# Kernel optimization log

Hardware: AMD Instinct MI355X
Metric: run time of the kernel (lower is better)

Reference implementation:

```python
import jax, jax.numpy as jnp
import numpy as np

B, S, D = 4, 2048, 1024
H, HD = 16, 64

def setup_inputs() -> dict:
    key = jax.random.key(0)
    ks = jax.random.split(key, 5)
    scale = 1.0 / np.sqrt(D)
    return {
        "x": jax.random.normal(ks[0], (B, S, D), dtype=jnp.float32),
        "Wq": jax.random.normal(ks[1], (D, D), dtype=jnp.float32) * scale,
        "Wk": jax.random.normal(ks[2], (D, D), dtype=jnp.float32) * scale,
        "Wv": jax.random.normal(ks[3], (D, D), dtype=jnp.float32) * scale,
        "Wo": jax.random.normal(ks[4], (D, D), dtype=jnp.float32) * scale,
        "bo": jnp.zeros((D,), dtype=jnp.float32),
    }

def reference(x, Wq, Wk, Wv, Wo, bo):
    batch, tokens, _ = x.shape
    # Linear weights applied as x @ W^T to match torch nn.Linear; here W is [out,in] equiv square
    q = (x @ Wq).reshape(batch, tokens, H, HD).transpose(0, 2, 1, 3)  # [B,H,S,HD]
    k = (x @ Wk).reshape(batch, tokens, H, HD).transpose(0, 2, 1, 3)
    v = (x @ Wv).reshape(batch, tokens, H, HD).transpose(0, 2, 1, 3)
    scores = jnp.einsum('bhqd,bhkd->bhqk', q, k) / jnp.sqrt(jnp.float32(HD))
    causal = jnp.tril(jnp.ones((tokens, tokens), dtype=bool))  # True = keep
    scores = jnp.where(causal[None, None], scores, -jnp.inf)
    attn = jax.nn.softmax(scores, axis=-1)  # dropout is identity (eval / rate 0)
    ctx = jnp.einsum('bhqk,bhkd->bhqd', attn, v)
    ctx = ctx.transpose(0, 2, 1, 3).reshape(batch, tokens, D)
    return ctx @ Wo + bo
```

## Files before the change

kernel.cpp:

```cpp
#include <hip/hip_runtime.h>
#include <math.h>
#include <stdint.h>

constexpr int kB = 4;
constexpr int kS = 2048;
constexpr int kD = 1024;
constexpr int kH = 16;
constexpr int kHD = 64;

typedef __bf16 bf16;
typedef __attribute__((ext_vector_type(4))) __bf16 bf16x4;
typedef __attribute__((ext_vector_type(8))) __bf16 bf16x8;
typedef __attribute__((ext_vector_type(4))) float f32x4;

__device__ __forceinline__ f32x4 mfma16x16x32(bf16x8 a, bf16x8 b, f32x4 c) {
    return __builtin_amdgcn_mfma_f32_16x16x32_bf16(a, b, c, 0, 0, 0);
}

#if __has_builtin(__builtin_amdgcn_exp2f)
#define EXP2F(x) __builtin_amdgcn_exp2f(x)
#else
#define EXP2F(x) exp2f(x)
#endif

__device__ __forceinline__ void load_lds16(const bf16* g, bf16* lds) {
    __builtin_amdgcn_global_load_lds(
        (const __attribute__((address_space(1))) void*)g,
        (__attribute__((address_space(3))) void*)lds, 16, 0, 0);
}

__global__ __launch_bounds__(256) void prep_x(const float* __restrict__ x,
                                              bf16* __restrict__ xb) {
    size_t i = ((size_t)blockIdx.x * 256 + threadIdx.x) * 8;
    float4 f0 = *(const float4*)(x + i);
    float4 f1 = *(const float4*)(x + i + 4);
    bf16x8 v;
    v[0] = (bf16)f0.x; v[1] = (bf16)f0.y; v[2] = (bf16)f0.z; v[3] = (bf16)f0.w;
    v[4] = (bf16)f1.x; v[5] = (bf16)f1.y; v[6] = (bf16)f1.z; v[7] = (bf16)f1.w;
    *(bf16x8*)(xb + i) = v;
}

__global__ __launch_bounds__(256) void prep_w(const float* __restrict__ Wq,
                                              const float* __restrict__ Wk,
                                              const float* __restrict__ Wv,
                                              const float* __restrict__ Wo,
                                              bf16* __restrict__ Wt) {
    __shared__ bf16 t[64 * 72];
    const int z = blockIdx.z;
    const float* W = (z == 0) ? Wq : (z == 1) ? Wk : (z == 2) ? Wv : Wo;
    const float scale = (z == 0) ? 0.18033688011112042f : 1.0f;
    const int k0 = blockIdx.x * 64, n0 = blockIdx.y * 64;
    const int tid = threadIdx.x;
    for (int p = 0; p < 16; ++p) {
        int idx = tid + p * 256;
        int r = idx >> 6, c = idx & 63;
        t[r * 72 + c] = (bf16)(W[(size_t)(k0 + r) * kD + n0 + c] * scale);
    }
    __syncthreads();
    for (int p = 0; p < 16; ++p) {
        int idx = tid + p * 256;
        int r = idx >> 6, c = idx & 63;
        Wt[(size_t)(z * 1024 + n0 + r) * kD + k0 + c] = t[c * 72 + r];
    }
}

__global__ __launch_bounds__(256) void qkv_gemm(
    const bf16* __restrict__ xb, const bf16* __restrict__ Wt,
    bf16* __restrict__ qo, bf16* __restrict__ ko, bf16* __restrict__ vto)
{
    __shared__ bf16 As[128 * 32];
    __shared__ bf16 Bs[128 * 32];

    const int tid  = threadIdx.x;
    const int wave = tid >> 6;
    const int lane = tid & 63;
    const int quad = lane >> 4;
    const int lr   = lane & 15;
    const int wm   = wave >> 1, wn = wave & 1;

    const int m0 = blockIdx.x * 128;
    const int n0 = blockIdx.y * 128;

    const int sr = tid >> 2, sc = tid & 3;

    f32x4 acc[4][4];
#pragma unroll
    for (int i = 0; i < 4; ++i)
#pragma unroll
        for (int nt = 0; nt < 4; ++nt) acc[i][nt] = f32x4{0.f, 0.f, 0.f, 0.f};

    for (int k0 = 0; k0 < kD; k0 += 32) {
        __syncthreads();
#pragma unroll
        for (int p = 0; p < 2; ++p) {
            int r = p * 64 + sr;
            load_lds16(&xb[(size_t)(m0 + r) * kD + k0 + sc * 8],
                       &As[(p * 256 + wave * 64) * 8]);
            load_lds16(&Wt[(size_t)(n0 + r) * kD + k0 + sc * 8],
                       &Bs[(p * 256 + wave * 64) * 8]);
        }
        __syncthreads();
        bf16x8 a[4], b[4];
#pragma unroll
        for (int i = 0; i < 4; ++i)
            a[i] = *(const bf16x8*)&As[(wm * 64 + i * 16 + lr) * 32 + quad * 8];
#pragma unroll
        for (int nt = 0; nt < 4; ++nt)
            b[nt] = *(const bf16x8*)&Bs[(wn * 64 + nt * 16 + lr) * 32 + quad * 8];
#pragma unroll
        for (int i = 0; i < 4; ++i)
#pragma unroll
            for (int nt = 0; nt < 4; ++nt)
                acc[i][nt] = mfma16x16x32(a[i], b[nt], acc[i][nt]);
    }

    const int w_idx = n0 >> 10;
    if (w_idx < 2) {
        bf16* dst = (w_idx == 0) ? qo : ko;
#pragma unroll
        for (int i = 0; i < 4; ++i)
#pragma unroll
            for (int nt = 0; nt < 4; ++nt) {
                int n   = n0 + wn * 64 + nt * 16 + lr;
                int col = n & 1023;
#pragma unroll
                for (int j = 0; j < 4; ++j) {
                    int m = m0 + wm * 64 + i * 16 + quad * 4 + j;
                    dst[(size_t)m * kD + col] = (bf16)acc[i][nt][j];
                }
            }
    } else {
#pragma unroll
        for (int i = 0; i < 4; ++i)
#pragma unroll
            for (int nt = 0; nt < 4; ++nt) {
                int n   = n0 + wn * 64 + nt * 16 + lr;
                int col = n & 1023, h = col >> 6, hd = col & 63;
                int mb  = m0 + wm * 64 + i * 16 + quad * 4;
                int b = mb >> 11, s = mb & 2047;
                bf16x4 pk;
#pragma unroll
                for (int j = 0; j < 4; ++j) pk[j] = (bf16)acc[i][nt][j];
                *(bf16x4*)&vto[((size_t)(b * kH + h) * kHD + hd) * kS + s] = pk;
            }
    }
}

__global__ __launch_bounds__(128, 2) void attn(
    const bf16* __restrict__ q, const bf16* __restrict__ k,
    const bf16* __restrict__ vt, bf16* __restrict__ ctx)
{
    __shared__ bf16 Ks[2][64 * 64];
    __shared__ bf16 Vs[2][64 * 64];
    __shared__ bf16 Pl[2][32 * 72];

    const int tid  = threadIdx.x;
    const int wave = tid >> 6;
    const int lane = tid & 63;
    const int quad = lane >> 4;
    const int lr   = lane & 15;

    const int bh = blockIdx.x;
    const int qb = gridDim.y - 1 - blockIdx.y;
    const int b  = bh >> 4;
    const int h  = bh & 15;

    const bf16* qb_p = q  + (size_t)b * kS * kD + h * kHD;
    const bf16* kb_p = k  + (size_t)b * kS * kD + h * kHD;
    const bf16* vt_p = vt + (size_t)bh * kHD * kS;

    const int T    = qb + 1;
    const int base = qb * 64 + wave * 32;

    const int grow   = lane >> 3;
    const int gchunk = ((lane & 7) ^ (grow & 7)) * 8;

    bf16x8 ones;
#pragma unroll
    for (int i = 0; i < 8; ++i) ones[i] = (bf16)1.0f;

    bf16x8 aq[2][2];
#pragma unroll
    for (int g = 0; g < 2; ++g)
#pragma unroll
        for (int kk = 0; kk < 2; ++kk)
            aq[g][kk] = *(const bf16x8*)&qb_p[(size_t)(base + g * 16 + lr) * kD + kk * 32 + quad * 8];

    f32x4 o[2][4];
    f32x4 lacc[2];
#pragma unroll
    for (int g = 0; g < 2; ++g) {
        lacc[g] = f32x4{0.f, 0.f, 0.f, 0.f};
#pragma unroll
        for (int nt = 0; nt < 4; ++nt) o[g][nt] = f32x4{0.f, 0.f, 0.f, 0.f};
    }

    bf16* Pw = &Pl[wave][0];

    if (wave == 0) {
#pragma unroll
        for (int i = 0; i < 8; ++i)
            load_lds16(kb_p + (size_t)(i * 8 + grow) * kD + gchunk, &Ks[0][i * 512]);
    } else {
#pragma unroll
        for (int i = 0; i < 8; ++i)
            load_lds16(vt_p + (size_t)(i * 8 + grow) * kS + gchunk, &Vs[0][i * 512]);
    }
    __syncthreads();

#pragma unroll 1
    for (int kt = 0; kt < T; ++kt) {
        const int k0  = kt * 64;
        const int buf = kt & 1;

        if (kt + 1 < T) {
            const int nk0 = k0 + 64;
            if (wave == 0) {
#pragma unroll
                for (int i = 0; i < 8; ++i)
                    load_lds16(kb_p + (size_t)(nk0 + i * 8 + grow) * kD + gchunk,
                               &Ks[buf ^ 1][i * 512]);
            } else {
#pragma unroll
                for (int i = 0; i < 8; ++i)
                    load_lds16(vt_p + (size_t)(i * 8 + grow) * kS + nk0 + gchunk,
                               &Vs[buf ^ 1][i * 512]);
            }
        }

        bf16x8 kf[4][2], vf[4][2];
#pragma unroll
        for (int nt = 0; nt < 4; ++nt)
#pragma unroll
            for (int kk = 0; kk < 2; ++kk) {
                const int sw = ((kk * 4 + quad) ^ (lr & 7)) << 3;
                kf[nt][kk] = *(const bf16x8*)&Ks[buf][(nt * 16 + lr) * 64 + sw];
                vf[nt][kk] = *(const bf16x8*)&Vs[buf][(nt * 16 + lr) * 64 + sw];
            }

        const bool lastt = (kt == T - 1);
#pragma unroll
        for (int g = 0; g < 2; ++g) {
            f32x4 sg[4];
            __builtin_amdgcn_s_setprio(1);
#pragma unroll
            for (int nt = 0; nt < 4; ++nt) {
                sg[nt] = mfma16x16x32(kf[nt][0], aq[g][0], f32x4{0.f, 0.f, 0.f, 0.f});
                sg[nt] = mfma16x16x32(kf[nt][1], aq[g][1], sg[nt]);
            }
            __builtin_amdgcn_s_setprio(0);
            if (lastt) {
                const int qg = base + g * 16 + lr;
#pragma unroll
                for (int nt = 0; nt < 4; ++nt) {
                    bf16x4 pk;
#pragma unroll
                    for (int j = 0; j < 4; ++j) {
                        float s = sg[nt][j];
                        s = (k0 + nt * 16 + quad * 4 + j > qg) ? -3.0e38f : s;
                        pk[j] = (bf16)EXP2F(s);
                    }
                    *(bf16x4*)&Pw[(g * 16 + lr) * 72 + nt * 16 + quad * 4] = pk;
                }
            } else {
#pragma unroll
                for (int nt = 0; nt < 4; ++nt) {
                    bf16x4 pk;
#pragma unroll
                    for (int j = 0; j < 4; ++j) pk[j] = (bf16)EXP2F(sg[nt][j]);
                    *(bf16x4*)&Pw[(g * 16 + lr) * 72 + nt * 16 + quad * 4] = pk;
                }
            }
        }

        __builtin_amdgcn_s_setprio(1);
#pragma unroll
        for (int g = 0; g < 2; ++g)
#pragma unroll
            for (int kk = 0; kk < 2; ++kk) {
                bf16x8 pa = *(const bf16x8*)&Pw[(g * 16 + lr) * 72 + kk * 32 + quad * 8];
                lacc[g] = mfma16x16x32(pa, ones, lacc[g]);
#pragma unroll
                for (int nt = 0; nt < 4; ++nt)
                    o[g][nt] = mfma16x16x32(pa, vf[nt][kk], o[g][nt]);
            }
        __builtin_amdgcn_s_setprio(0);

        __syncthreads();
    }

#pragma unroll
    for (int g = 0; g < 2; ++g) {
        float inv[4];
#pragma unroll
        for (int j = 0; j < 4; ++j) inv[j] = 1.0f / lacc[g][j];
#pragma unroll
        for (int nt = 0; nt < 4; ++nt) {
            int hd = nt * 16 + lr;
#pragma unroll
            for (int j = 0; j < 4; ++j) {
                int qg = base + g * 16 + quad * 4 + j;
                ctx[((size_t)(b * kS + qg)) * kD + h * kHD + hd] = (bf16)(o[g][nt][j] * inv[j]);
            }
        }
    }
}

__global__ __launch_bounds__(256) void out_gemm(
    const bf16* __restrict__ ctxb, const bf16* __restrict__ Wto,
    const float* __restrict__ bo, float* __restrict__ out)
{
    __shared__ bf16 As[128 * 32];
    __shared__ bf16 Bs[128 * 32];

    const int tid  = threadIdx.x;
    const int wave = tid >> 6;
    const int lane = tid & 63;
    const int quad = lane >> 4;
    const int lr   = lane & 15;
    const int wm   = wave >> 1, wn = wave & 1;

    const int m0 = blockIdx.x * 128;
    const int n0 = blockIdx.y * 128;

    const int sr = tid >> 2, sc = tid & 3;

    f32x4 acc[4][4];
#pragma unroll
    for (int i = 0; i < 4; ++i)
#pragma unroll
        for (int nt = 0; nt < 4; ++nt) acc[i][nt] = f32x4{0.f, 0.f, 0.f, 0.f};

    for (int k0 = 0; k0 < kD; k0 += 32) {
        __syncthreads();
#pragma unroll
        for (int p = 0; p < 2; ++p) {
            int r = p * 64 + sr;
            load_lds16(&ctxb[(size_t)(m0 + r) * kD + k0 + sc * 8],
                       &As[(p * 256 + wave * 64) * 8]);
            load_lds16(&Wto[(size_t)(n0 + r) * kD + k0 + sc * 8],
                       &Bs[(p * 256 + wave * 64) * 8]);
        }
        __syncthreads();
        bf16x8 a[4], b[4];
#pragma unroll
        for (int i = 0; i < 4; ++i)
            a[i] = *(const bf16x8*)&As[(wm * 64 + i * 16 + lr) * 32 + quad * 8];
#pragma unroll
        for (int nt = 0; nt < 4; ++nt)
            b[nt] = *(const bf16x8*)&Bs[(wn * 64 + nt * 16 + lr) * 32 + quad * 8];
#pragma unroll
        for (int i = 0; i < 4; ++i)
#pragma unroll
            for (int nt = 0; nt < 4; ++nt)
                acc[i][nt] = mfma16x16x32(a[i], b[nt], acc[i][nt]);
    }

#pragma unroll
    for (int nt = 0; nt < 4; ++nt) {
        int n = n0 + wn * 64 + nt * 16 + lr;
        float bias = bo[n];
#pragma unroll
        for (int i = 0; i < 4; ++i)
#pragma unroll
            for (int j = 0; j < 4; ++j) {
                int m = m0 + wm * 64 + i * 16 + quad * 4 + j;
                out[(size_t)m * kD + n] = acc[i][nt][j] + bias;
            }
    }
}

extern "C" void kernel_launch(void* const* d_in, const int* in_sizes, int n_in,
                              void* d_out, int out_size, void* d_ws, size_t ws_size,
                              hipStream_t stream) {
    const float* x  = (const float*)d_in[0];
    const float* Wq = (const float*)d_in[1];
    const float* Wk = (const float*)d_in[2];
    const float* Wv = (const float*)d_in[3];
    const float* Wo = (const float*)d_in[4];
    const float* bo = (const float*)d_in[5];
    float* out = (float*)d_out;

    const size_t n_x   = (size_t)kB * kS * kD;
    const size_t n_w   = (size_t)4 * kD * kD;
    const size_t n_mat = (size_t)kB * kH * kS * kHD;

    bf16* xb  = (bf16*)d_ws;
    bf16* Wt  = xb + n_x;
    bf16* Qm  = Wt + n_w;
    bf16* Km  = Qm + n_mat;
    bf16* Vt  = Km + n_mat;
    bf16* ctx = xb;

    prep_x<<<dim3((int)(n_x / (256 * 8))), dim3(256), 0, stream>>>(x, xb);
    prep_w<<<dim3(16, 16, 4), dim3(256), 0, stream>>>(Wq, Wk, Wv, Wo, Wt);
    qkv_gemm<<<dim3(8192 / 128, 3072 / 128), dim3(256), 0, stream>>>(xb, Wt, Qm, Km, Vt);
    attn<<<dim3(kB * kH, 32), dim3(128), 0, stream>>>(Qm, Km, Vt, ctx);
    out_gemm<<<dim3(8192 / 128, 1024 / 128), dim3(256), 0, stream>>>(
        ctx, Wt + (size_t)3 * kD * kD, bo, out);
}
```

Baseline: 248.4 us.

## Split attention query tile across four waves of 16 rows each

The attention kernel now launches 256 threads per block, and each of the four waves handles 16 query rows instead of two waves handling 32 rows each. Only waves 0 and 1 still issue the K and V tile loads into shared memory; the other two waves only compute. Per-wave register use roughly halves (one group of accumulators), so more waves can run concurrently and latency hiding should improve. The trade-off is that each K/V fragment read from LDS now feeds fewer MFMAs per wave, which adds LDS read traffic relative to compute.

```diff
diff --git a/kernel.cpp b/kernel.cpp
--- a/kernel.cpp
+++ b/kernel.cpp
@@ -146,13 +146,13 @@
     }
 }
 
-__global__ __launch_bounds__(128, 2) void attn(
+__global__ __launch_bounds__(256, 3) void attn(
     const bf16* __restrict__ q, const bf16* __restrict__ k,
     const bf16* __restrict__ vt, bf16* __restrict__ ctx)
 {
     __shared__ bf16 Ks[2][64 * 64];
     __shared__ bf16 Vs[2][64 * 64];
-    __shared__ bf16 Pl[2][32 * 72];
+    __shared__ bf16 Pl[4][16 * 72];
 
     const int tid  = threadIdx.x;
     const int wave = tid >> 6;
@@ -170,7 +170,7 @@
     const bf16* vt_p = vt + (size_t)bh * kHD * kS;
 
     const int T    = qb + 1;
-    const int base = qb * 64 + wave * 32;
+    const int base = qb * 64 + wave * 16;
 
     const int grow   = lane >> 3;
     const int gchunk = ((lane & 7) ^ (grow & 7)) * 8;
@@ -179,21 +179,15 @@
 #pragma unroll
     for (int i = 0; i < 8; ++i) ones[i] = (bf16)1.0f;
 
-    bf16x8 aq[2][2];
-#pragma unroll
-    for (int g = 0; g < 2; ++g)
-#pragma unroll
-        for (int kk = 0; kk < 2; ++kk)
-            aq[g][kk] = *(const bf16x8*)&qb_p[(size_t)(base + g * 16 + lr) * kD + kk * 32 + quad * 8];
-
-    f32x4 o[2][4];
-    f32x4 lacc[2];
-#pragma unroll
-    for (int g = 0; g < 2; ++g) {
-        lacc[g] = f32x4{0.f, 0.f, 0.f, 0.f};
-#pragma unroll
-        for (int nt = 0; nt < 4; ++nt) o[g][nt] = f32x4{0.f, 0.f, 0.f, 0.f};
-    }
+    bf16x8 aq[2];
+#pragma unroll
+    for (int kk = 0; kk < 2; ++kk)
+        aq[kk] = *(const bf16x8*)&qb_p[(size_t)(base + lr) * kD + kk * 32 + quad * 8];
+
+    f32x4 o[4];
+    f32x4 lacc = f32x4{0.f, 0.f, 0.f, 0.f};
+#pragma unroll
+    for (int nt = 0; nt < 4; ++nt) o[nt] = f32x4{0.f, 0.f, 0.f, 0.f};
 
     bf16* Pw = &Pl[wave][0];
 
@@ -201,7 +195,7 @@
 #pragma unroll
         for (int i = 0; i < 8; ++i)
             load_lds16(kb_p + (size_t)(i * 8 + grow) * kD + gchunk, &Ks[0][i * 512]);
-    } else {
+    } else if (wave == 1) {
 #pragma unroll
         for (int i = 0; i < 8; ++i)
             load_lds16(vt_p + (size_t)(i * 8 + grow) * kS + gchunk, &Vs[0][i * 512]);
@@ -220,7 +214,7 @@
                 for (int i = 0; i < 8; ++i)
                     load_lds16(kb_p + (size_t)(nk0 + i * 8 + grow) * kD + gchunk,
                                &Ks[buf ^ 1][i * 512]);
-            } else {
+            } else if (wave == 1) {
 #pragma unroll
                 for (int i = 0; i < 8; ++i)
                     load_lds16(vt_p + (size_t)(i * 8 + grow) * kS + nk0 + gchunk,
@@ -238,70 +232,62 @@
                 vf[nt][kk] = *(const bf16x8*)&Vs[buf][(nt * 16 + lr) * 64 + sw];
             }
 
-        const bool lastt = (kt == T - 1);
-#pragma unroll
-        for (int g = 0; g < 2; ++g) {
-            f32x4 sg[4];
-            __builtin_amdgcn_s_setprio(1);
+        f32x4 sg[4];
+        __builtin_amdgcn_s_setprio(1);
+#pragma unroll
+        for (int nt = 0; nt < 4; ++nt) {
+            sg[nt] = mfma16x16x32(kf[nt][0], aq[0], f32x4{0.f, 0.f, 0.f, 0.f});
+            sg[nt] = mfma16x16x32(kf[nt][1], aq[1], sg[nt]);
+        }
+        __builtin_amdgcn_s_setprio(0);
+
+        if (kt == T - 1) {
+            const int qg = base + lr;
 #pragma unroll
             for (int nt = 0; nt < 4; ++nt) {
-                sg[nt] = mfma16x16x32(kf[nt][0], aq[g][0], f32x4{0.f, 0.f, 0.f, 0.f});
-                sg[nt] = mfma16x16x32(kf[nt][1], aq[g][1], sg[nt]);
-            }
-            __builtin_amdgcn_s_setprio(0);
-            if (lastt) {
-                const int qg = base + g * 16 + lr;
-#pragma unroll
-                for (int nt = 0; nt < 4; ++nt) {
-                    bf16x4 pk;
-#pragma unroll
-                    for (int j = 0; j < 4; ++j) {
-                        float s = sg[nt][j];
-                        s = (k0 + nt * 16 + quad * 4 + j > qg) ? -3.0e38f : s;
-                        pk[j] = (bf16)EXP2F(s);
-                    }
-                    *(bf16x4*)&Pw[(g * 16 + lr) * 72 + nt * 16 + quad * 4] = pk;
+                bf16x4 pk;
+#pragma unroll
+                for (int j = 0; j < 4; ++j) {
+                    float s = sg[nt][j];
+                    s = (k0 + nt * 16 + quad * 4 + j > qg) ? -3.0e38f : s;
+                    pk[j] = (bf16)EXP2F(s);
                 }
-            } else {
-#pragma unroll
-                for (int nt = 0; nt < 4; ++nt) {
-                    bf16x4 pk;
-#pragma unroll
-                    for (int j = 0; j < 4; ++j) pk[j] = (bf16)EXP2F(sg[nt][j]);
-                    *(bf16x4*)&Pw[(g * 16 + lr) * 72 + nt * 16 + quad * 4] = pk;
-                }
+                *(bf16x4*)&Pw[lr * 72 + nt * 16 + quad * 4] = pk;
+            }
+        } else {
+#pragma unroll
+            for (int nt = 0; nt < 4; ++nt) {
+                bf16x4 pk;
+#pragma unroll
+                for (int j = 0; j < 4; ++j) pk[j] = (bf16)EXP2F(sg[nt][j]);
+                *(bf16x4*)&Pw[lr * 72 + nt * 16 + quad * 4] = pk;
             }
         }
 
         __builtin_amdgcn_s_setprio(1);
 #pragma unroll
-        for (int g = 0; g < 2; ++g)
-#pragma unroll
-            for (int kk = 0; kk < 2; ++kk) {
-                bf16x8 pa = *(const bf16x8*)&Pw[(g * 16 + lr) * 72 + kk * 32 + quad * 8];
-                lacc[g] = mfma16x16x32(pa, ones, lacc[g]);
-#pragma unroll
-                for (int nt = 0; nt < 4; ++nt)
-                    o[g][nt] = mfma16x16x32(pa, vf[nt][kk], o[g][nt]);
-            }
+        for (int kk = 0; kk < 2; ++kk) {
+            bf16x8 pa = *(const bf16x8*)&Pw[lr * 72 + kk * 32 + quad * 8];
+            lacc = mfma16x16x32(pa, ones, lacc);
+#pragma unroll
+            for (int nt = 0; nt < 4; ++nt)
+                o[nt] = mfma16x16x32(pa, vf[nt][kk], o[nt]);
+        }
         __builtin_amdgcn_s_setprio(0);
 
         __syncthreads();
     }
 
-#pragma unroll
-    for (int g = 0; g < 2; ++g) {
-        float inv[4];
-#pragma unroll
-        for (int j = 0; j < 4; ++j) inv[j] = 1.0f / lacc[g][j];
-#pragma unroll
-        for (int nt = 0; nt < 4; ++nt) {
-            int hd = nt * 16 + lr;
-#pragma unroll
-            for (int j = 0; j < 4; ++j) {
-                int qg = base + g * 16 + quad * 4 + j;
-                ctx[((size_t)(b * kS + qg)) * kD + h * kHD + hd] = (bf16)(o[g][nt][j] * inv[j]);
-            }
+    float inv[4];
+#pragma unroll
+    for (int j = 0; j < 4; ++j) inv[j] = 1.0f / lacc[j];
+#pragma unroll
+    for (int nt = 0; nt < 4; ++nt) {
+        int hd = nt * 16 + lr;
+#pragma unroll
+        for (int j = 0; j < 4; ++j) {
+            int qg = base + quad * 4 + j;
+            ctx[((size_t)(b * kS + qg)) * kD + h * kHD + hd] = (bf16)(o[nt][j] * inv[j]);
         }
     }
 }
@@ -395,7 +381,7 @@
     prep_x<<<dim3((int)(n_x / (256 * 8))), dim3(256), 0, stream>>>(x, xb);
     prep_w<<<dim3(16, 16, 4), dim3(256), 0, stream>>>(Wq, Wk, Wv, Wo, Wt);
     qkv_gemm<<<dim3(8192 / 128, 3072 / 128), dim3(256), 0, stream>>>(xb, Wt, Qm, Km, Vt);
-    attn<<<dim3(kB * kH, 32), dim3(128), 0, stream>>>(Qm, Km, Vt, ctx);
+    attn<<<dim3(kB * kH, 32), dim3(256), 0, stream>>>(Qm, Km, Vt, ctx);
     out_gemm<<<dim3(8192 / 128, 1024 / 128), dim3(256), 0, stream>>>(
         ctx, Wt + (size_t)3 * kD * kD, bo, out);
 }
```

Result: faster. 239.9 us (-3.4%).
